# Kernel optimization log

Hardware: AMD Instinct MI355X
Metric: run time of the kernel (lower is better)

Reference implementation:

```python
import jax, jax.numpy as jnp
import numpy as np

N, E, D, L = 100000, 640000, 128, 5
BN_EPS = 1e-5


def setup_inputs() -> dict:
    key = jax.random.key(0)
    ks = jax.random.split(key, 10)
    x = jax.random.normal(ks[0], (N, D), jnp.float32)
    edge_index = jax.random.randint(ks[1], (2, E), 0, N, dtype=jnp.int32)
    W1 = jax.random.normal(ks[2], (L, D, 2 * D), jnp.float32) / np.float32(np.sqrt(D))
    b1 = jnp.zeros((L, 2 * D), jnp.float32)
    bn1_g = jnp.ones((L, 2 * D), jnp.float32)
    bn1_b = jnp.zeros((L, 2 * D), jnp.float32)
    bn1_m = 0.1 * jax.random.normal(ks[3], (L, 2 * D), jnp.float32)
    bn1_v = jax.random.uniform(ks[4], (L, 2 * D), jnp.float32) + 0.5
    W2 = jax.random.normal(ks[5], (L, 2 * D, D), jnp.float32) / np.float32(np.sqrt(2 * D))
    b2 = jnp.zeros((L, D), jnp.float32)
    bno_g = jnp.ones((L, D), jnp.float32)
    bno_b = jnp.zeros((L, D), jnp.float32)
    bno_m = 0.1 * jax.random.normal(ks[6], (L, D), jnp.float32)
    bno_v = jax.random.uniform(ks[7], (L, D), jnp.float32) + 0.5
    return {"x": x, "edge_index": edge_index, "W1": W1, "b1": b1,
            "bn1_g": bn1_g, "bn1_b": bn1_b, "bn1_m": bn1_m, "bn1_v": bn1_v,
            "W2": W2, "b2": b2,
            "bno_g": bno_g, "bno_b": bno_b, "bno_m": bno_m, "bno_v": bno_v}


def _bn(z, g, b, m, v):
    # BatchNorm1d in eval mode: running stats
    return (z - m) * jax.lax.rsqrt(v + BN_EPS) * g + b


def reference(x, edge_index, W1, b1, bn1_g, bn1_b, bn1_m, bn1_v,
              W2, b2, bno_g, bno_b, bno_m, bno_v):
    src, dst = edge_index[0], edge_index[1]
    h = x
    for l in range(L):
        # GINConv with eps=0: (1+eps)*h_i + sum_{j->i} h_j
        agg = h + jax.ops.segment_sum(h[src], dst, num_segments=N)  # [N, d]
        z = jax.nn.relu(_bn(agg @ W1[l] + b1[l], bn1_g[l], bn1_b[l], bn1_m[l], bn1_v[l]))
        h = _bn(z @ W2[l] + b2[l], bno_g[l], bno_b[l], bno_m[l], bno_v[l])
        if l != L - 1:
            h = jax.nn.relu(h)
        # dropout is identity in eval mode
    return h
```

## Files before the change

kernel.cpp:

```cpp
#include <hip/hip_runtime.h>

#define ND 100000
#define DD 128
#define HH 256
#define EE 640000
#define LL 5

#define GS 152
#define ZS 280

typedef __attribute__((ext_vector_type(8))) short short8;
typedef __attribute__((ext_vector_type(4))) short short4v;
typedef __attribute__((ext_vector_type(4))) float f32x4;
typedef __attribute__((ext_vector_type(8))) _Float16 half8;
typedef __attribute__((ext_vector_type(4))) _Float16 half4;
typedef __attribute__((ext_vector_type(2))) _Float16 half2v;

static __device__ __forceinline__ short f2h(float f) {
    return __builtin_bit_cast(short, (_Float16)f);
}

static __device__ __forceinline__ half2v pk2(float a, float b) {
    return __builtin_bit_cast(half2v, __builtin_amdgcn_cvt_pkrtz(a, b));
}

__global__ __launch_bounds__(256) void setup(
    const float* __restrict__ W1, const float* __restrict__ b1,
    const float* __restrict__ g1, const float* __restrict__ bb1,
    const float* __restrict__ m1, const float* __restrict__ v1,
    const float* __restrict__ W2, const float* __restrict__ b2,
    const float* __restrict__ g2, const float* __restrict__ bb2,
    const float* __restrict__ m2, const float* __restrict__ v2,
    const float* __restrict__ x, const int* __restrict__ dst,
    short* __restrict__ W1p, float* __restrict__ b1e,
    short* __restrict__ W2p, float* __restrict__ b2e,
    short* __restrict__ hb, int* __restrict__ cnt)
{
    int bx = blockIdx.x;
    int tid = threadIdx.x;
    if (bx < 640) {
        int id = bx * 256 + tid;
        if (id < LL * HH * DD) {
            int l = id >> 15;
            int rem = id & 32767;
            {
                int n = rem >> 7, k = rem & 127;
                float s = g1[l * HH + n] * rsqrtf(v1[l * HH + n] + 1e-5f);
                W1p[id] = f2h(W1[l * 32768 + k * HH + n] * s);
            }
            {
                int n2 = rem >> 8, k2 = rem & 255;
                float s = g2[l * DD + n2] * rsqrtf(v2[l * DD + n2] + 1e-5f);
                W2p[id] = f2h(W2[l * 32768 + k2 * DD + n2] * s);
            }
        }
        if (id < LL * HH) {
            float s = g1[id] * rsqrtf(v1[id] + 1e-5f);
            b1e[id] = (b1[id] - m1[id]) * s + bb1[id];
        }
        if (id < LL * DD) {
            float s = g2[id] * rsqrtf(v2[id] + 1e-5f);
            b2e[id] = (b2[id] - m2[id]) * s + bb2[id];
        }
    } else if (bx < 13140) {
        int i = (bx - 640) * 256 + tid;
        float4 v = reinterpret_cast<const float4*>(x)[i];
        half2v p0 = pk2(v.x, v.y);
        half2v p1 = pk2(v.z, v.w);
        half4 hv = __builtin_shufflevector(p0, p1, 0, 1, 2, 3);
        reinterpret_cast<short4v*>(hb)[i] = __builtin_bit_cast(short4v, hv);
    } else {
        int e = (bx - 13140) * 256 + tid;
        if (e < EE) atomicAdd(&cnt[dst[e]], 1);
    }
}

__global__ __launch_bounds__(256) void scan_block(int* __restrict__ cnt, int* __restrict__ bsum)
{
    __shared__ int buf[256];
    int tid = threadIdx.x;
    int idx = blockIdx.x * 256 + tid;
    int v = (idx < ND) ? cnt[idx] : 0;
    buf[tid] = v;
    __syncthreads();
    int sum = v;
    for (int off = 1; off < 256; off <<= 1) {
        int t = (tid >= off) ? buf[tid - off] : 0;
        __syncthreads();
        sum += t;
        buf[tid] = sum;
        __syncthreads();
    }
    if (idx < ND) cnt[idx] = sum;
    if (tid == 255) bsum[blockIdx.x] = sum;
}

__global__ __launch_bounds__(256) void apply_offs2(const int* __restrict__ cnt,
                                                   const int* __restrict__ bsum,
                                                   int* __restrict__ rowst)
{
    __shared__ int sred[256];
    int tid = threadIdx.x;
    int partial = 0;
    for (int i = tid; i < blockIdx.x; i += 256) partial += bsum[i];
    sred[tid] = partial;
    __syncthreads();
    for (int off = 128; off > 0; off >>= 1) {
        if (tid < off) sred[tid] += sred[tid + off];
        __syncthreads();
    }
    int boff = sred[0];
    int idx = blockIdx.x * 256 + tid;
    if (idx < ND) rowst[idx + 1] = cnt[idx] + boff;
    if (idx == 0) rowst[0] = 0;
}

__global__ __launch_bounds__(256) void fill_csr(const int* __restrict__ src,
                                                const int* __restrict__ dst,
                                                const int* __restrict__ rowstart,
                                                int* __restrict__ cursor,
                                                int* __restrict__ csr)
{
    int e = blockIdx.x * 256 + threadIdx.x;
    if (e < EE) {
        int d = dst[e];
        int p = atomicAdd(&cursor[d], 1);
        csr[rowstart[d] + p] = src[e];
    }
}

__global__ __launch_bounds__(1024, 8) void layer_fused(
    const short* __restrict__ hb_in,
    const int* __restrict__ rowst,
    const int* __restrict__ csr,
    const short* __restrict__ W1l,
    const float* __restrict__ b1l,
    const short* __restrict__ W2l,
    const float* __restrict__ b2l,
    short* __restrict__ hb_out, float* __restrict__ f_out, int last)
{
    __shared__ __attribute__((aligned(16))) short sU[64 * ZS];

    const int tid = threadIdx.x;
    const int r0 = blockIdx.x * 64;
    const int wave = tid >> 6;
    const int lane = tid & 63;
    const int quad = lane >> 4;
    const int l16 = lane & 15;

    {
        int row = tid >> 4;
        int ch = (tid & 15) * 8;
        int grow = r0 + row;
        const int gbase = lane & 48;
        half8 acc = {};
        if (grow < ND) {
            acc = __builtin_bit_cast(half8,
                *reinterpret_cast<const short8*>(&hb_in[(size_t)grow * DD + ch]));
            int s = rowst[grow], e = rowst[grow + 1];
            int deg = e - s;
            int i = s;
            while (deg > 0) {
                int myidx = csr[i + (tid & 15)];
                int c = deg < 16 ? deg : 16;
                int done = 0;
                while (done < c) {
                    int cc = c - done; if (cc > 8) cc = 8;
                    half8 a[8];
                    #pragma unroll
                    for (int k = 0; k < 8; ++k) {
                        if (k < cc) {
                            int srcrow = __shfl(myidx, gbase + done + k, 64);
                            a[k] = __builtin_bit_cast(half8,
                                *reinterpret_cast<const short8*>(
                                    &hb_in[(size_t)srcrow * DD + ch]));
                        }
                    }
                    #pragma unroll
                    for (int k = 0; k < 8; ++k)
                        if (k < cc) acc = acc + a[k];
                    done += cc;
                }
                i += c; deg -= c;
            }
        }
        *reinterpret_cast<short8*>(&sU[row * GS + ch]) = __builtin_bit_cast(short8, acc);
    }

    const int zrow = wave * 16 + l16;
    half8 aw1[4];
    for (int ks = 0; ks < 4; ++ks)
        aw1[ks] = __builtin_bit_cast(half8,
            *reinterpret_cast<const short8*>(&W1l[zrow * DD + ks * 32 + quad * 8]));
    float4 bias1 = *reinterpret_cast<const float4*>(&b1l[wave * 16 + quad * 4]);
    __syncthreads();

    const f32x4 zero4 = {0.f, 0.f, 0.f, 0.f};
    f32x4 acc1[4];
    for (int nt = 0; nt < 4; ++nt) acc1[nt] = zero4;

    for (int ks = 0; ks < 4; ++ks) {
        int kofs = ks * 32 + quad * 8;
        for (int nt = 0; nt < 4; ++nt) {
            half8 bn = __builtin_bit_cast(half8,
                *reinterpret_cast<const short8*>(&sU[(nt * 16 + l16) * GS + kofs]));
            acc1[nt] = __builtin_amdgcn_mfma_f32_16x16x32_f16(aw1[ks], bn, acc1[nt], 0, 0, 0);
        }
    }
    __syncthreads();

    {
        int zc = wave * 16 + quad * 4;
        for (int nt = 0; nt < 4; ++nt) {
            int node = nt * 16 + l16;
            half2v p0 = pk2(fmaxf(acc1[nt][0] + bias1.x, 0.f),
                            fmaxf(acc1[nt][1] + bias1.y, 0.f));
            half2v p1 = pk2(fmaxf(acc1[nt][2] + bias1.z, 0.f),
                            fmaxf(acc1[nt][3] + bias1.w, 0.f));
            half4 hv = __builtin_shufflevector(p0, p1, 0, 1, 2, 3);
            *reinterpret_cast<short4v*>(&sU[node * ZS + zc]) = __builtin_bit_cast(short4v, hv);
        }
    }

    const int ct16 = wave >> 1;
    const int nh = wave & 1;
    const int orow = ct16 * 16 + l16;
    half8 w_cur = __builtin_bit_cast(half8,
        *reinterpret_cast<const short8*>(&W2l[orow * HH + quad * 8]));
    float4 bias2 = *reinterpret_cast<const float4*>(&b2l[ct16 * 16 + quad * 4]);
    __syncthreads();

    f32x4 acc2[2];
    for (int nt = 0; nt < 2; ++nt) acc2[nt] = zero4;

    for (int ks = 0; ks < 8; ++ks) {
        half8 w_next;
        if (ks < 7)
            w_next = __builtin_bit_cast(half8,
                *reinterpret_cast<const short8*>(&W2l[orow * HH + (ks + 1) * 32 + quad * 8]));
        int kofs = ks * 32 + quad * 8;
        for (int nt = 0; nt < 2; ++nt) {
            int node = nh * 32 + nt * 16 + l16;
            half8 bn = __builtin_bit_cast(half8,
                *reinterpret_cast<const short8*>(&sU[node * ZS + kofs]));
            acc2[nt] = __builtin_amdgcn_mfma_f32_16x16x32_f16(w_cur, bn, acc2[nt], 0, 0, 0);
        }
        w_cur = w_next;
    }

    {
        int oc = ct16 * 16 + quad * 4;
        for (int nt = 0; nt < 2; ++nt) {
            int node = r0 + nh * 32 + nt * 16 + l16;
            if (node < ND) {
                float v0 = acc2[nt][0] + bias2.x;
                float v1 = acc2[nt][1] + bias2.y;
                float v2 = acc2[nt][2] + bias2.z;
                float v3 = acc2[nt][3] + bias2.w;
                if (!last) {
                    half2v p0 = pk2(fmaxf(v0, 0.f), fmaxf(v1, 0.f));
                    half2v p1 = pk2(fmaxf(v2, 0.f), fmaxf(v3, 0.f));
                    half4 hv = __builtin_shufflevector(p0, p1, 0, 1, 2, 3);
                    *reinterpret_cast<short4v*>(&hb_out[(size_t)node * DD + oc]) =
                        __builtin_bit_cast(short4v, hv);
                } else {
                    float4 st; st.x = v0; st.y = v1; st.z = v2; st.w = v3;
                    *reinterpret_cast<float4*>(&f_out[(size_t)node * DD + oc]) = st;
                }
            }
        }
    }
}

extern "C" void kernel_launch(void* const* d_in, const int* in_sizes, int n_in,
                              void* d_out, int out_size, void* d_ws, size_t ws_size,
                              hipStream_t stream)
{
    const float* x  = (const float*)d_in[0];
    const int* ei   = (const int*)d_in[1];
    const int* src  = ei;
    const int* dst  = ei + EE;
    const float* W1 = (const float*)d_in[2];
    const float* b1 = (const float*)d_in[3];
    const float* g1 = (const float*)d_in[4];
    const float* bb1= (const float*)d_in[5];
    const float* m1 = (const float*)d_in[6];
    const float* v1 = (const float*)d_in[7];
    const float* W2 = (const float*)d_in[8];
    const float* b2 = (const float*)d_in[9];
    const float* g2 = (const float*)d_in[10];
    const float* bb2= (const float*)d_in[11];
    const float* m2 = (const float*)d_in[12];
    const float* v2 = (const float*)d_in[13];

    char* w = (char*)d_ws;
    short* hbufA = (short*)w;
    short* hbufB = (short*)(w + 25600000);
    short* W1p   = (short*)(w + 51200000);
    short* W2p   = (short*)(w + 51527680);
    float* b1e   = (float*)(w + 51855360);
    float* b2e   = (float*)(w + 51860480);
    int*   cnt   = (int*)  (w + 51863040);
    int*   cursor= (int*)  (w + 52263040);
    int*   rowst = (int*)  (w + 52663040);
    int*   csr   = (int*)  (w + 53063072);
    int*   bsum  = (int*)  (w + 55623136);
    float* out   = (float*)d_out;

    (void)hipMemsetAsync(cnt, 0, 800000, stream);
    setup<<<15640, 256, 0, stream>>>(W1, b1, g1, bb1, m1, v1,
                                     W2, b2, g2, bb2, m2, v2,
                                     x, dst, W1p, b1e, W2p, b2e, hbufA, cnt);
    scan_block<<<391, 256, 0, stream>>>(cnt, bsum);
    apply_offs2<<<391, 256, 0, stream>>>(cnt, bsum, rowst);
    fill_csr<<<2500, 256, 0, stream>>>(src, dst, rowst, cursor, csr);

    short* hin = hbufA;
    short* hout = hbufB;
    for (int l = 0; l < LL; ++l) {
        layer_fused<<<1563, 1024, 0, stream>>>(hin, rowst, csr,
                                               W1p + l * 32768, b1e + l * HH,
                                               W2p + l * 32768, b2e + l * DD,
                                               hout, out, (l == LL - 1) ? 1 : 0);
        short* t = hin; hin = hout; hout = t;
    }
}
```

Measured before the change: 534.0 us.

## Split fused GIN layer into separate gather-aggregate and MLP kernels

Moves the CSR neighbor gather-sum out of the fused layer kernel into its own 256-thread kernel that writes the aggregated fp16 features to a global buffer, which the MLP kernel then reads. The aim is to let the latency-bound irregular gather run at higher occupancy, without the 1024-thread LDS-heavy blocks and the GEMM stage stalled behind it. The cost is an extra global write and read of the N×128 fp16 aggregate per layer and one more launch per layer. The MLP now writes its output back in place into the single h buffer, which is safe because the gather has already finished.

After: 582.8 us. 1.09x slower.

```diff
diff --git a/kernel.cpp b/kernel.cpp
--- a/kernel.cpp
+++ b/kernel.cpp
@@ -129,10 +129,39 @@
     }
 }
 
-__global__ __launch_bounds__(1024, 8) void layer_fused(
+__global__ __launch_bounds__(256) void gather_agg(
     const short* __restrict__ hb_in,
     const int* __restrict__ rowst,
     const int* __restrict__ csr,
+    short* __restrict__ aggb)
+{
+    const int row = blockIdx.x * 16 + (threadIdx.x >> 4);
+    const int ch = (threadIdx.x & 15) * 8;
+    if (row >= ND) return;
+
+    half8 acc = __builtin_bit_cast(half8,
+        *reinterpret_cast<const short8*>(&hb_in[(size_t)row * DD + ch]));
+    int i = rowst[row];
+    int deg = rowst[row + 1] - i;
+    while (deg > 0) {
+        int c = deg < 8 ? deg : 8;
+        half8 a[8];
+        #pragma unroll
+        for (int k = 0; k < 8; ++k)
+            if (k < c)
+                a[k] = __builtin_bit_cast(half8,
+                    *reinterpret_cast<const short8*>(&hb_in[(size_t)csr[i + k] * DD + ch]));
+        #pragma unroll
+        for (int k = 0; k < 8; ++k)
+            if (k < c) acc = acc + a[k];
+        i += c; deg -= c;
+    }
+    *reinterpret_cast<short8*>(&aggb[(size_t)row * DD + ch]) =
+        __builtin_bit_cast(short8, acc);
+}
+
+__global__ __launch_bounds__(1024, 8) void mlp(
+    const short* __restrict__ aggb,
     const short* __restrict__ W1l,
     const float* __restrict__ b1l,
     const short* __restrict__ W2l,
@@ -152,39 +181,10 @@
         int row = tid >> 4;
         int ch = (tid & 15) * 8;
         int grow = r0 + row;
-        const int gbase = lane & 48;
-        half8 acc = {};
-        if (grow < ND) {
-            acc = __builtin_bit_cast(half8,
-                *reinterpret_cast<const short8*>(&hb_in[(size_t)grow * DD + ch]));
-            int s = rowst[grow], e = rowst[grow + 1];
-            int deg = e - s;
-            int i = s;
-            while (deg > 0) {
-                int myidx = csr[i + (tid & 15)];
-                int c = deg < 16 ? deg : 16;
-                int done = 0;
-                while (done < c) {
-                    int cc = c - done; if (cc > 8) cc = 8;
-                    half8 a[8];
-                    #pragma unroll
-                    for (int k = 0; k < 8; ++k) {
-                        if (k < cc) {
-                            int srcrow = __shfl(myidx, gbase + done + k, 64);
-                            a[k] = __builtin_bit_cast(half8,
-                                *reinterpret_cast<const short8*>(
-                                    &hb_in[(size_t)srcrow * DD + ch]));
-                        }
-                    }
-                    #pragma unroll
-                    for (int k = 0; k < 8; ++k)
-                        if (k < cc) acc = acc + a[k];
-                    done += cc;
-                }
-                i += c; deg -= c;
-            }
-        }
-        *reinterpret_cast<short8*>(&sU[row * GS + ch]) = __builtin_bit_cast(short8, acc);
+        short8 v = {};
+        if (grow < ND)
+            v = *reinterpret_cast<const short8*>(&aggb[(size_t)grow * DD + ch]);
+        *reinterpret_cast<short8*>(&sU[row * GS + ch]) = v;
     }
 
     const int zrow = wave * 16 + l16;
@@ -294,8 +294,8 @@
     const float* v2 = (const float*)d_in[13];
 
     char* w = (char*)d_ws;
-    short* hbufA = (short*)w;
-    short* hbufB = (short*)(w + 25600000);
+    short* hbuf  = (short*)w;
+    short* aggb  = (short*)(w + 25600000);
     short* W1p   = (short*)(w + 51200000);
     short* W2p   = (short*)(w + 51527680);
     float* b1e   = (float*)(w + 51855360);
@@ -310,18 +310,16 @@
     (void)hipMemsetAsync(cnt, 0, 800000, stream);
     setup<<<15640, 256, 0, stream>>>(W1, b1, g1, bb1, m1, v1,
                                      W2, b2, g2, bb2, m2, v2,
-                                     x, dst, W1p, b1e, W2p, b2e, hbufA, cnt);
+                                     x, dst, W1p, b1e, W2p, b2e, hbuf, cnt);
     scan_block<<<391, 256, 0, stream>>>(cnt, bsum);
     apply_offs2<<<391, 256, 0, stream>>>(cnt, bsum, rowst);
     fill_csr<<<2500, 256, 0, stream>>>(src, dst, rowst, cursor, csr);
 
-    short* hin = hbufA;
-    short* hout = hbufB;
     for (int l = 0; l < LL; ++l) {
-        layer_fused<<<1563, 1024, 0, stream>>>(hin, rowst, csr,
-                                               W1p + l * 32768, b1e + l * HH,
-                                               W2p + l * 32768, b2e + l * DD,
-                                               hout, out, (l == LL - 1) ? 1 : 0);
-        short* t = hin; hin = hout; hout = t;
-    }
-}
+        gather_agg<<<6250, 256, 0, stream>>>(hbuf, rowst, csr, aggb);
+        mlp<<<1563, 1024, 0, stream>>>(aggb,
+                                       W1p + l * 32768, b1e + l * HH,
+                                       W2p + l * 32768, b2e + l * DD,
+                                       hbuf, out, (l == LL - 1) ? 1 : 0);
+    }
+}
```

## Process two 64-node tiles per block, overlapping second gather with first tile's GEMMs

Applied to the files above, without the earlier changes.

Each block now handles 128 nodes in two halves. The neighbor gather for the second half is issued (first four neighbors prefetched) and finished around the first half's MLP matrix work, so memory latency overlaps MFMA compute. W1 fragments loaded into registers are reused across both halves. The gather loop also drops the wave-shuffle index broadcast in favour of direct csr reads per thread. Separate LDS buffers for the gathered features and the hidden activations raise shared memory per block, which could lower occupancy, and the block count halves.

After: 595.4 us. 1.11x slower.

```diff
diff --git a/kernel.cpp b/kernel.cpp
--- a/kernel.cpp
+++ b/kernel.cpp
@@ -139,53 +139,17 @@
     const float* __restrict__ b2l,
     short* __restrict__ hb_out, float* __restrict__ f_out, int last)
 {
-    __shared__ __attribute__((aligned(16))) short sU[64 * ZS];
+    __shared__ __attribute__((aligned(16))) short sG[64 * GS];
+    __shared__ __attribute__((aligned(16))) short sZ[64 * ZS];
 
     const int tid = threadIdx.x;
-    const int r0 = blockIdx.x * 64;
+    const int r0 = blockIdx.x * 128;
     const int wave = tid >> 6;
     const int lane = tid & 63;
     const int quad = lane >> 4;
     const int l16 = lane & 15;
-
-    {
-        int row = tid >> 4;
-        int ch = (tid & 15) * 8;
-        int grow = r0 + row;
-        const int gbase = lane & 48;
-        half8 acc = {};
-        if (grow < ND) {
-            acc = __builtin_bit_cast(half8,
-                *reinterpret_cast<const short8*>(&hb_in[(size_t)grow * DD + ch]));
-            int s = rowst[grow], e = rowst[grow + 1];
-            int deg = e - s;
-            int i = s;
-            while (deg > 0) {
-                int myidx = csr[i + (tid & 15)];
-                int c = deg < 16 ? deg : 16;
-                int done = 0;
-                while (done < c) {
-                    int cc = c - done; if (cc > 8) cc = 8;
-                    half8 a[8];
-                    #pragma unroll
-                    for (int k = 0; k < 8; ++k) {
-                        if (k < cc) {
-                            int srcrow = __shfl(myidx, gbase + done + k, 64);
-                            a[k] = __builtin_bit_cast(half8,
-                                *reinterpret_cast<const short8*>(
-                                    &hb_in[(size_t)srcrow * DD + ch]));
-                        }
-                    }
-                    #pragma unroll
-                    for (int k = 0; k < 8; ++k)
-                        if (k < cc) acc = acc + a[k];
-                    done += cc;
-                }
-                i += c; deg -= c;
-            }
-        }
-        *reinterpret_cast<short8*>(&sU[row * GS + ch]) = __builtin_bit_cast(short8, acc);
-    }
+    const int row = tid >> 4;
+    const int ch = (tid & 15) * 8;
 
     const int zrow = wave * 16 + l16;
     half8 aw1[4];
@@ -193,17 +157,58 @@
         aw1[ks] = __builtin_bit_cast(half8,
             *reinterpret_cast<const short8*>(&W1l[zrow * DD + ks * 32 + quad * 8]));
     float4 bias1 = *reinterpret_cast<const float4*>(&b1l[wave * 16 + quad * 4]);
-    __syncthreads();
+
+    {
+        int grow = r0 + row;
+        half8 acc = {};
+        if (grow < ND) {
+            acc = __builtin_bit_cast(half8,
+                *reinterpret_cast<const short8*>(&hb_in[(size_t)grow * DD + ch]));
+            int i = rowst[grow];
+            int deg = rowst[grow + 1] - i;
+            while (deg > 0) {
+                int c = deg < 8 ? deg : 8;
+                half8 a[8];
+                #pragma unroll
+                for (int k = 0; k < 8; ++k)
+                    if (k < c)
+                        a[k] = __builtin_bit_cast(half8,
+                            *reinterpret_cast<const short8*>(&hb_in[(size_t)csr[i + k] * DD + ch]));
+                #pragma unroll
+                for (int k = 0; k < 8; ++k)
+                    if (k < c) acc = acc + a[k];
+                i += c; deg -= c;
+            }
+        }
+        *reinterpret_cast<short8*>(&sG[row * GS + ch]) = __builtin_bit_cast(short8, acc);
+    }
+    __syncthreads();
+
+    const int grow1 = r0 + 64 + row;
+    int s1 = 0, deg1 = 0, c1 = 0;
+    half8 h1 = {};
+    half8 p1[4];
+    if (grow1 < ND) {
+        s1 = rowst[grow1];
+        deg1 = rowst[grow1 + 1] - s1;
+        h1 = __builtin_bit_cast(half8,
+            *reinterpret_cast<const short8*>(&hb_in[(size_t)grow1 * DD + ch]));
+        c1 = deg1 < 4 ? deg1 : 4;
+        #pragma unroll
+        for (int k = 0; k < 4; ++k)
+            if (k < c1)
+                p1[k] = __builtin_bit_cast(half8,
+                    *reinterpret_cast<const short8*>(&hb_in[(size_t)csr[s1 + k] * DD + ch]));
+    }
 
     const f32x4 zero4 = {0.f, 0.f, 0.f, 0.f};
     f32x4 acc1[4];
     for (int nt = 0; nt < 4; ++nt) acc1[nt] = zero4;
-
     for (int ks = 0; ks < 4; ++ks) {
         int kofs = ks * 32 + quad * 8;
         for (int nt = 0; nt < 4; ++nt) {
             half8 bn = __builtin_bit_cast(half8,
-                *reinterpret_cast<const short8*>(&sU[(nt * 16 + l16) * GS + kofs]));
+                *reinterpret_cast<const short8*>(&sG[(nt * 16 + l16) * GS + kofs]));
             acc1[nt] = __builtin_amdgcn_mfma_f32_16x16x32_f16(aw1[ks], bn, acc1[nt], 0, 0, 0);
         }
     }
@@ -215,11 +220,35 @@
             int node = nt * 16 + l16;
             half2v p0 = pk2(fmaxf(acc1[nt][0] + bias1.x, 0.f),
                             fmaxf(acc1[nt][1] + bias1.y, 0.f));
-            half2v p1 = pk2(fmaxf(acc1[nt][2] + bias1.z, 0.f),
+            half2v q1 = pk2(fmaxf(acc1[nt][2] + bias1.z, 0.f),
                             fmaxf(acc1[nt][3] + bias1.w, 0.f));
-            half4 hv = __builtin_shufflevector(p0, p1, 0, 1, 2, 3);
-            *reinterpret_cast<short4v*>(&sU[node * ZS + zc]) = __builtin_bit_cast(short4v, hv);
-        }
+            half4 hv = __builtin_shufflevector(p0, q1, 0, 1, 2, 3);
+            *reinterpret_cast<short4v*>(&sZ[node * ZS + zc]) = __builtin_bit_cast(short4v, hv);
+        }
+    }
+    {
+        half8 acc = h1;
+        #pragma unroll
+        for (int k = 0; k < 4; ++k)
+            if (k < c1) acc = acc + p1[k];
+        if (grow1 < ND) {
+            int i = s1 + c1;
+            int deg = deg1 - c1;
+            while (deg > 0) {
+                int c = deg < 8 ? deg : 8;
+                half8 a[8];
+                #pragma unroll
+                for (int k = 0; k < 8; ++k)
+                    if (k < c)
+                        a[k] = __builtin_bit_cast(half8,
+                            *reinterpret_cast<const short8*>(&hb_in[(size_t)csr[i + k] * DD + ch]));
+                #pragma unroll
+                for (int k = 0; k < 8; ++k)
+                    if (k < c) acc = acc + a[k];
+                i += c; deg -= c;
+            }
+        }
+        *reinterpret_cast<short8*>(&sG[row * GS + ch]) = __builtin_bit_cast(short8, acc);
     }
 
     const int ct16 = wave >> 1;
@@ -231,8 +260,7 @@
     __syncthreads();
 
     f32x4 acc2[2];
-    for (int nt = 0; nt < 2; ++nt) acc2[nt] = zero4;
-
+    acc2[0] = zero4; acc2[1] = zero4;
     for (int ks = 0; ks < 8; ++ks) {
         half8 w_next;
         if (ks < 7)
@@ -242,10 +270,21 @@
         for (int nt = 0; nt < 2; ++nt) {
             int node = nh * 32 + nt * 16 + l16;
             half8 bn = __builtin_bit_cast(half8,
-                *reinterpret_cast<const short8*>(&sU[node * ZS + kofs]));
+                *reinterpret_cast<const short8*>(&sZ[node * ZS + kofs]));
             acc2[nt] = __builtin_amdgcn_mfma_f32_16x16x32_f16(w_cur, bn, acc2[nt], 0, 0, 0);
         }
         w_cur = w_next;
+    }
+
+    f32x4 acc1b[4];
+    for (int nt = 0; nt < 4; ++nt) acc1b[nt] = zero4;
+    for (int ks = 0; ks < 4; ++ks) {
+        int kofs = ks * 32 + quad * 8;
+        for (int nt = 0; nt < 4; ++nt) {
+            half8 bn = __builtin_bit_cast(half8,
+                *reinterpret_cast<const short8*>(&sG[(nt * 16 + l16) * GS + kofs]));
+            acc1b[nt] = __builtin_amdgcn_mfma_f32_16x16x32_f16(aw1[ks], bn, acc1b[nt], 0, 0, 0);
+        }
     }
 
     {
@@ -259,8 +298,64 @@
                 float v3 = acc2[nt][3] + bias2.w;
                 if (!last) {
                     half2v p0 = pk2(fmaxf(v0, 0.f), fmaxf(v1, 0.f));
-                    half2v p1 = pk2(fmaxf(v2, 0.f), fmaxf(v3, 0.f));
-                    half4 hv = __builtin_shufflevector(p0, p1, 0, 1, 2, 3);
+                    half2v q1 = pk2(fmaxf(v2, 0.f), fmaxf(v3, 0.f));
+                    half4 hv = __builtin_shufflevector(p0, q1, 0, 1, 2, 3);
+                    *reinterpret_cast<short4v*>(&hb_out[(size_t)node * DD + oc]) =
+                        __builtin_bit_cast(short4v, hv);
+                } else {
+                    float4 st; st.x = v0; st.y = v1; st.z = v2; st.w = v3;
+                    *reinterpret_cast<float4*>(&f_out[(size_t)node * DD + oc]) = st;
+                }
+            }
+        }
+    }
+    __syncthreads();
+
+    {
+        int zc = wave * 16 + quad * 4;
+        for (int nt = 0; nt < 4; ++nt) {
+            int node = nt * 16 + l16;
+            half2v p0 = pk2(fmaxf(acc1b[nt][0] + bias1.x, 0.f),
+                            fmaxf(acc1b[nt][1] + bias1.y, 0.f));
+            half2v q1 = pk2(fmaxf(acc1b[nt][2] + bias1.z, 0.f),
+                            fmaxf(acc1b[nt][3] + bias1.w, 0.f));
+            half4 hv = __builtin_shufflevector(p0, q1, 0, 1, 2, 3);
+            *reinterpret_cast<short4v*>(&sZ[node * ZS + zc]) = __builtin_bit_cast(short4v, hv);
+        }
+    }
+    half8 w_cur2 = __builtin_bit_cast(half8,
+        *reinterpret_cast<const short8*>(&W2l[orow * HH + quad * 8]));
+    __syncthreads();
+
+    f32x4 acc2b[2];
+    acc2b[0] = zero4; acc2b[1] = zero4;
+    for (int ks = 0; ks < 8; ++ks) {
+        half8 w_next;
+        if (ks < 7)
+            w_next = __builtin_bit_cast(half8,
+                *reinterpret_cast<const short8*>(&W2l[orow * HH + (ks + 1) * 32 + quad * 8]));
+        int kofs = ks * 32 + quad * 8;
+        for (int nt = 0; nt < 2; ++nt) {
+            int node = nh * 32 + nt * 16 + l16;
+            half8 bn = __builtin_bit_cast(half8,
+                *reinterpret_cast<const short8*>(&sZ[node * ZS + kofs]));
+            acc2b[nt] = __builtin_amdgcn_mfma_f32_16x16x32_f16(w_cur2, bn, acc2b[nt], 0, 0, 0);
+        }
+        w_cur2 = w_next;
+    }
+    {
+        int oc = ct16 * 16 + quad * 4;
+        for (int nt = 0; nt < 2; ++nt) {
+            int node = r0 + 64 + nh * 32 + nt * 16 + l16;
+            if (node < ND) {
+                float v0 = acc2b[nt][0] + bias2.x;
+                float v1 = acc2b[nt][1] + bias2.y;
+                float v2 = acc2b[nt][2] + bias2.z;
+                float v3 = acc2b[nt][3] + bias2.w;
+                if (!last) {
+                    half2v p0 = pk2(fmaxf(v0, 0.f), fmaxf(v1, 0.f));
+                    half2v q1 = pk2(fmaxf(v2, 0.f), fmaxf(v3, 0.f));
+                    half4 hv = __builtin_shufflevector(p0, q1, 0, 1, 2, 3);
                     *reinterpret_cast<short4v*>(&hb_out[(size_t)node * DD + oc]) =
                         __builtin_bit_cast(short4v, hv);
                 } else {
@@ -318,10 +413,10 @@
     short* hin = hbufA;
     short* hout = hbufB;
     for (int l = 0; l < LL; ++l) {
-        layer_fused<<<1563, 1024, 0, stream>>>(hin, rowst, csr,
-                                               W1p + l * 32768, b1e + l * HH,
-                                               W2p + l * 32768, b2e + l * DD,
-                                               hout, out, (l == LL - 1) ? 1 : 0);
+        layer_fused<<<782, 1024, 0, stream>>>(hin, rowst, csr,
+                                              W1p + l * 32768, b1e + l * HH,
+                                              W2p + l * 32768, b2e + l * DD,
+                                              hout, out, (l == LL - 1) ? 1 : 0);
         short* t = hin; hin = hout; hout = t;
     }
 }
```
